# Kernel tuning notes

Hardware: AMD Instinct MI355X
Metric: run time of the kernel (lower is better)

## Reference

```python
import jax, jax.numpy as jnp
import numpy as np

SCALES = (128.0, 256.0, 512.0)
ASPECT = (0.5, 1.0, 2.0)
K = 9
NMS_THR = 0.7
PRE_NMS_TOPK = 10000
POST_NMS_TOPK = 2000
MIN_SIZE = 16.0

def conv2d(x, w, b, pad):
    out = jax.lax.conv_general_dilated(x, w, (1, 1), [(pad, pad), (pad, pad)], dimension_numbers=('NCHW', 'OIHW', 'NCHW'))
    return out + b[None, :, None, None]

def generate_anchors(grid_h, grid_w, dtype):
    # Faithful to source: shifts are grid indices, NOT multiplied by stride (source bug kept).
    scales = jnp.asarray(SCALES, dtype)
    ar = jnp.asarray(ASPECT, dtype)
    h_ratio = jnp.sqrt(ar)
    w_ratio = 1.0 / h_ratio
    ws = (w_ratio[:, None] * scales[None, :]).reshape(-1)
    hs = (h_ratio[:, None] * scales[None, :]).reshape(-1)
    base = jnp.round(jnp.stack([-ws, -hs, ws, hs], axis=1) / 2.0)  # (9,4)
    sy, sx = jnp.meshgrid(jnp.arange(grid_h), jnp.arange(grid_w), indexing='ij')
    sx = sx.reshape(-1).astype(dtype)
    sy = sy.reshape(-1).astype(dtype)
    shifts = jnp.stack([sx, sy, sx, sy], axis=1)  # (H*W,4)
    return (shifts[:, None, :] + base[None, :, :]).reshape(-1, 4)  # (H*W*9,4)

def decode(box_pred, anchors):
    w = anchors[:, 2] - anchors[:, 0]
    h = anchors[:, 3] - anchors[:, 1]
    cx = anchors[:, 0] + 0.5 * w
    cy = anchors[:, 1] + 0.5 * h
    dx, dy, dw, dh = box_pred[:, 0], box_pred[:, 1], box_pred[:, 2], box_pred[:, 3]
    pcx = dx * w + cx
    pcy = dy * h + cy
    pw = jnp.exp(dw) * w
    ph = jnp.exp(dh) * h
    return jnp.stack([pcx - 0.5 * pw, pcy - 0.5 * ph, pcx + 0.5 * pw, pcy + 0.5 * ph], axis=1)

def nms_keep(boxes, valid, thr):
    # Greedy NMS on score-descending boxes; invalid (small) boxes never kept nor suppress others.
    n = boxes.shape[0]
    x1, y1, x2, y2 = boxes[:, 0], boxes[:, 1], boxes[:, 2], boxes[:, 3]
    areas = (x2 - x1) * (y2 - y1)
    idx = jnp.arange(n)
    def body(i, keep):
        xx1 = jnp.maximum(x1, x1[i]); yy1 = jnp.maximum(y1, y1[i])
        xx2 = jnp.minimum(x2, x2[i]); yy2 = jnp.minimum(y2, y2[i])
        inter = jnp.maximum(xx2 - xx1, 0.0) * jnp.maximum(yy2 - yy1, 0.0)
        iou = inter / (areas + areas[i] - inter)
        suppress = (iou > thr) & (idx > i) & keep[i]
        return keep & (~suppress)
    return jax.lax.fori_loop(0, n, body, valid)

def filter_proposals(proposals, cls_scores, img_h, img_w):
    scores = jax.nn.sigmoid(cls_scores.reshape(-1))
    top_scores, top_idx = jax.lax.top_k(scores, PRE_NMS_TOPK)  # sorted descending
    props = proposals[top_idx]
    x1 = jnp.clip(props[:, 0], 0.0, img_w); y1 = jnp.clip(props[:, 1], 0.0, img_h)
    x2 = jnp.clip(props[:, 2], 0.0, img_w); y2 = jnp.clip(props[:, 3], 0.0, img_h)
    props = jnp.stack([x1, y1, x2, y2], axis=1)
    valid = ((x2 - x1) >= MIN_SIZE) & ((y2 - y1) >= MIN_SIZE)
    keep = jax.lax.stop_gradient(nms_keep(jax.lax.stop_gradient(props), valid, NMS_THR))
    masked = jnp.where(keep, top_scores, -1.0)
    final_scores, final_idx = jax.lax.top_k(masked, POST_NMS_TOPK)  # order = score-descending (matches post-NMS sort)
    final_props = props[final_idx]
    valid_out = final_scores > 0.0  # sigmoid scores > 0, padding = -1
    return jnp.where(valid_out[:, None], final_props, 0.0), jnp.where(valid_out, final_scores, 0.0)

def setup_inputs():
    key = jax.random.key(0)
    ks = jax.random.split(key, 8)
    C = 512; GH = GW = 50
    feat = jax.random.normal(ks[0], (1, C, GH, GW), jnp.float32)
    image = jnp.zeros((1, 3, 800, 800), jnp.float32)
    gt_boxes = jax.random.uniform(ks[1], (8, 4), jnp.float32) * 800.0
    w_rpn = jax.random.normal(ks[2], (C, C, 3, 3), jnp.float32) * 0.01
    b_rpn = jnp.zeros((C,), jnp.float32)
    w_cls = jax.random.normal(ks[3], (K, C, 1, 1), jnp.float32) * 0.01
    b_cls = jnp.zeros((K,), jnp.float32)
    w_reg = jax.random.normal(ks[4], (4 * K, C, 1, 1), jnp.float32) * 0.01
    b_reg = jnp.zeros((4 * K,), jnp.float32)
    return {"image": image, "feat": feat, "gt_boxes": gt_boxes, "w_rpn": w_rpn, "b_rpn": b_rpn, "w_cls": w_cls, "b_cls": b_cls, "w_reg": w_reg, "b_reg": b_reg}

def reference(image, feat, gt_boxes, w_rpn, b_rpn, w_cls, b_cls, w_reg, b_reg):
    rpn_feat = jax.nn.relu(conv2d(feat, w_rpn, b_rpn, 1))
    cls = conv2d(rpn_feat, w_cls, b_cls, 0)      # (B,9,H,W)
    reg = conv2d(rpn_feat, w_reg, b_reg, 0)      # (B,36,H,W)
    B, _, gh, gw = feat.shape
    anchors = generate_anchors(gh, gw, feat.dtype)
    # flatten to anchor ordering (h, w, k) matching generate_anchors
    cls_flat = jnp.transpose(cls, (0, 2, 3, 1)).reshape(-1)
    reg_flat = jnp.transpose(reg.reshape(B, K, 4, gh, gw), (0, 3, 4, 1, 2)).reshape(-1, 4)
    proposals = decode(reg_flat, anchors)
    img_h, img_w = float(image.shape[-2]), float(image.shape[-1])
    return filter_proposals(proposals, cls_flat, img_h, img_w)
```

## Files before the change

### kernel.cpp

```cpp
#include <hip/hip_runtime.h>
#include <cmath>
#include <cstdint>
#include <cstddef>

typedef unsigned long long u64;
typedef unsigned int u32;

#define NPX   2500
#define NANCH 22500
#define PRE_TOPK 10000
#define NWORDS 160

struct AnchorBase { float b[36]; };

typedef __attribute__((ext_vector_type(8))) short bf16x8;
typedef __attribute__((ext_vector_type(4))) float f32x4;

__device__ inline unsigned short f2bf(float f) {
    u32 u = __float_as_uint(f);
    u32 r = u + 0x7fffu + ((u >> 16) & 1u);
    return (unsigned short)(r >> 16);
}
__device__ inline float bf2f(unsigned short h) {
    return __uint_as_float(((u32)h) << 16);
}

__global__ __launch_bounds__(256) void kprep(const float* __restrict__ feat,
                                             const float* __restrict__ wr,
                                             unsigned short* __restrict__ xthi,
                                             unsigned short* __restrict__ xtlo,
                                             unsigned short* __restrict__ whi,
                                             unsigned short* __restrict__ wlo)
{
    __shared__ float sh[4608];
    int bid = blockIdx.x;
    int t = threadIdx.x;
    if (bid < 416) {
        float (*tile)[65] = (float(*)[65])sh;
        int gr = bid >> 3;
        int cc = bid & 7;
        int tx = t & 63, ty = t >> 6;
        int y = gr - 1;
        bool rowok = (gr >= 1) && (gr <= 50);
#pragma unroll
        for (int i = 0; i < 16; ++i) {
            int c = i * 4 + ty;
            tile[c][tx] = (rowok && tx < 50)
                        ? feat[(size_t)(cc * 64 + c) * NPX + y * 50 + tx] : 0.f;
        }
        __syncthreads();
#pragma unroll
        for (int i = 0; i < 16; ++i) {
            int xp = i * 4 + ty;
            int cell = gr * 64 + xp;
            bool ok = rowok && xp >= 1 && xp <= 50;
            float v = ok ? tile[tx][xp - 1] : 0.f;
            unsigned short hi = f2bf(v);
            xthi[(size_t)cell * 512 + cc * 64 + tx] = hi;
            xtlo[(size_t)cell * 512 + cc * 64 + tx] = f2bf(v - bf2f(hi));
        }
    } else {
        int oc = bid - 416;
        for (int j = t; j < 4608; j += 256) sh[j] = wr[(size_t)oc * 4608 + j];
        __syncthreads();
        for (int k = t; k < 4608; k += 256) {
            int c = k & 511, tap = k >> 9;
            float v = sh[c * 9 + tap];
            unsigned short hi = f2bf(v);
            whi[(size_t)oc * 4608 + k] = hi;
            wlo[(size_t)oc * 4608 + k] = f2bf(v - bf2f(hi));
        }
    }
}

__global__ __launch_bounds__(256) void k1m(const unsigned short* __restrict__ xthi,
                                           const unsigned short* __restrict__ xtlo,
                                           const unsigned short* __restrict__ whi,
                                           const unsigned short* __restrict__ wlo,
                                           float* __restrict__ pk,
                                           int cptLog, int cptm1, int cptMul, int niter)
{
    __shared__ __align__(16) unsigned short Ah[8192];
    __shared__ __align__(16) unsigned short Al[8192];
    __shared__ __align__(16) unsigned short Bh[4096];
    __shared__ __align__(16) unsigned short Bl[4096];

    int t = threadIdx.x;
    int lane = t & 63, wave = t >> 6;
    int wo = wave & 1, wp = wave >> 1;
    int ocb = blockIdx.x, pxb = blockIdx.y, bs = blockIdx.z;
    int q = lane >> 4, m = lane & 15;
    int c0base = bs * cptMul;

    int g  = t & 7;
    int r0 = t >> 3;
    int ocA[4];
    int cellB[2];
#pragma unroll
    for (int i = 0; i < 4; ++i) ocA[i] = ocb * 128 + r0 + 32 * i;
#pragma unroll
    for (int i = 0; i < 2; ++i) {
        int opx = pxb * 64 + r0 + 32 * i;
        cellB[i] = (opx < NPX) ? ((opx / 50) + 1) * 64 + (opx % 50) + 1 : 190;
    }

    f32x4 acc[8];
    f32x4 zf = {0.f, 0.f, 0.f, 0.f};
#pragma unroll
    for (int i = 0; i < 8; ++i) acc[i] = zf;

    for (int it = 0; it < niter; ++it) {
        int tap = it >> cptLog;
        int cw  = it & cptm1;
        int c0  = c0base + cw * 64;
        int t3  = (tap * 43) >> 7;
        int tapoff = (t3 - 1) * 64 + (tap - t3 * 3) - 1;
#pragma unroll
        for (int i = 0; i < 4; ++i) {
            int rl = r0 + 32 * i;
            int la = rl * 64 + g * 8;
            size_t ga = (size_t)ocA[i] * 4608 + tap * 512 + c0 + g * 8;
            *(bf16x8*)(Ah + la) = *(const bf16x8*)(whi + ga);
            *(bf16x8*)(Al + la) = *(const bf16x8*)(wlo + ga);
        }
#pragma unroll
        for (int i = 0; i < 2; ++i) {
            int rl = r0 + 32 * i;
            int la = rl * 64 + g * 8;
            size_t gb = (size_t)(cellB[i] + tapoff) * 512 + c0 + g * 8;
            *(bf16x8*)(Bh + la) = *(const bf16x8*)(xthi + gb);
            *(bf16x8*)(Bl + la) = *(const bf16x8*)(xtlo + gb);
        }
        __syncthreads();
#pragma unroll
        for (int ks = 0; ks < 2; ++ks) {
            bf16x8 fah[4], fal[4], fbh[2], fbl[2];
#pragma unroll
            for (int mt = 0; mt < 4; ++mt) {
                int off = (wo * 64 + mt * 16 + m) * 64 + ks * 32 + q * 8;
                fah[mt] = *(const bf16x8*)(Ah + off);
                fal[mt] = *(const bf16x8*)(Al + off);
            }
#pragma unroll
            for (int nt = 0; nt < 2; ++nt) {
                int off = (wp * 32 + nt * 16 + m) * 64 + ks * 32 + q * 8;
                fbh[nt] = *(const bf16x8*)(Bh + off);
                fbl[nt] = *(const bf16x8*)(Bl + off);
            }
#pragma unroll
            for (int mt = 0; mt < 4; ++mt)
#pragma unroll
                for (int nt = 0; nt < 2; ++nt) {
                    f32x4 a = acc[mt * 2 + nt];
                    a = __builtin_amdgcn_mfma_f32_16x16x32_bf16(fal[mt], fbh[nt], a, 0, 0, 0);
                    a = __builtin_amdgcn_mfma_f32_16x16x32_bf16(fah[mt], fbl[nt], a, 0, 0, 0);
                    a = __builtin_amdgcn_mfma_f32_16x16x32_bf16(fah[mt], fbh[nt], a, 0, 0, 0);
                    acc[mt * 2 + nt] = a;
                }
        }
        __syncthreads();
    }
#pragma unroll
    for (int mt = 0; mt < 4; ++mt)
#pragma unroll
        for (int nt = 0; nt < 2; ++nt)
#pragma unroll
            for (int r = 0; r < 4; ++r) {
                int oc = ocb * 128 + wo * 64 + mt * 16 + q * 4 + r;
                int px = pxb * 64 + wp * 32 + nt * 16 + m;
                pk[((size_t)bs * 512 + oc) * 2560 + px] = acc[mt * 2 + nt][r];
            }
}

__global__ __launch_bounds__(256) void k2a_heads(const float* __restrict__ pk, int ns,
                                                 const float* __restrict__ br,
                                                 const float* __restrict__ wcls,
                                                 const float* __restrict__ wreg,
                                                 float* __restrict__ part)
{
    __shared__ float vt[64 * 64];
    __shared__ float Wl[45 * 64];
    int t  = threadIdx.x;
    int pb = blockIdx.x;
    int s  = blockIdx.y;
    int cb = s * 64;
    for (int e = t; e < 45 * 64; e += 256) {
        int u = e >> 6, c = e & 63;
        Wl[e] = (u < 9) ? wcls[u * 512 + cb + c] : wreg[(u - 9) * 512 + cb + c];
    }
    int pxl = t & 63, ug = t >> 6;
    int px = pb * 64 + pxl;
    bool ok = px < NPX;
#pragma unroll
    for (int i = 0; i < 16; ++i) {
        int c = ug * 16 + i;
        float v = 0.f;
        if (ok) {
            size_t bidx = (size_t)(cb + c) * 2560 + px;
            v = br[cb + c];
            for (int ks = 0; ks < ns; ++ks) v += pk[(size_t)ks * 512 * 2560 + bidx];
            v = v > 0.f ? v : 0.f;
        }
        vt[c * 64 + pxl] = v;
    }
    __syncthreads();
    int ubase = ug * 12;
    int ulim  = (45 - ubase < 12) ? (45 - ubase) : 12;
    float acc[12];
#pragma unroll
    for (int j = 0; j < 12; ++j) acc[j] = 0.f;
    for (int c = 0; c < 64; ++c) {
        float v = vt[c * 64 + pxl];
#pragma unroll
        for (int j = 0; j < 12; ++j)
            acc[j] = fmaf(v, Wl[(ubase + j) * 64 + c], acc[j]);
    }
    if (ok) {
        for (int j = 0; j < ulim; ++j)
            part[((size_t)s * 45 + ubase + j) * NPX + px] = acc[j];
    }
}

__global__ __launch_bounds__(256) void k2b_decode(const float* __restrict__ part,
                                                  const float* __restrict__ bcls,
                                                  const float* __restrict__ breg,
                                                  AnchorBase ab,
                                                  float* __restrict__ score,
                                                  float* __restrict__ bx1, float* __restrict__ by1,
                                                  float* __restrict__ bx2, float* __restrict__ by2,
                                                  u32* __restrict__ valid,
                                                  u64* __restrict__ key)
{
    int id = blockIdx.x * 256 + threadIdx.x;
    if (id >= NANCH) return;
    int k  = id / NPX;
    int px = id - k * NPX;

    float z  = bcls[k];
    float d0 = breg[k * 4 + 0], d1 = breg[k * 4 + 1];
    float d2 = breg[k * 4 + 2], d3 = breg[k * 4 + 3];
#pragma unroll
    for (int s = 0; s < 8; ++s) {
        const float* p = part + (size_t)s * 45 * NPX;
        z  += p[(size_t)k * NPX + px];
        d0 += p[(size_t)(9 + k * 4 + 0) * NPX + px];
        d1 += p[(size_t)(9 + k * 4 + 1) * NPX + px];
        d2 += p[(size_t)(9 + k * 4 + 2) * NPX + px];
        d3 += p[(size_t)(9 + k * 4 + 3) * NPX + px];
    }
    float sc = 1.f / (1.f + expf(-z));

    int yy = px / 50, xx = px - (px / 50) * 50;
    float fx = (float)xx, fy = (float)yy;
    float ax1 = fx + ab.b[k * 4 + 0], ay1 = fy + ab.b[k * 4 + 1];
    float ax2 = fx + ab.b[k * 4 + 2], ay2 = fy + ab.b[k * 4 + 3];
    float aw = ax2 - ax1, ah = ay2 - ay1;
    float cx = ax1 + 0.5f * aw, cy = ay1 + 0.5f * ah;
    float pcx = d0 * aw + cx, pcy = d1 * ah + cy;
    float pw = expf(d2) * aw, ph = expf(d3) * ah;
    float x1 = pcx - 0.5f * pw, y1 = pcy - 0.5f * ph;
    float x2 = pcx + 0.5f * pw, y2 = pcy + 0.5f * ph;
    x1 = fminf(fmaxf(x1, 0.f), 800.f);
    y1 = fminf(fmaxf(y1, 0.f), 800.f);
    x2 = fminf(fmaxf(x2, 0.f), 800.f);
    y2 = fminf(fmaxf(y2, 0.f), 800.f);
    u32 v = ((x2 - x1) >= 16.f) && ((y2 - y1) >= 16.f);

    int f = px * 9 + k;
    score[f] = sc;
    bx1[f] = x1; by1[f] = y1; bx2[f] = x2; by2[f] = y2;
    valid[f] = v;
    u32 sb = __float_as_uint(sc);
    key[f] = ((u64)(~sb) << 32) | (u32)f;
}

__global__ __launch_bounds__(256) void k3a_rank(const u64* __restrict__ key,
                                                u32* __restrict__ rankp)
{
    __shared__ __align__(16) u64 sk[2250];
    int t  = threadIdx.x;
    int jb = blockIdx.y;
    for (int e = t; e < 2250; e += 256) sk[e] = key[jb * 2250 + e];
    __syncthreads();
    int i0 = blockIdx.x * 1024 + t;
    int i1 = i0 + 256, i2 = i0 + 512, i3 = i0 + 768;
    u64 k0 = (i0 < NANCH) ? key[i0] : 0ull;
    u64 k1 = (i1 < NANCH) ? key[i1] : 0ull;
    u64 k2 = (i2 < NANCH) ? key[i2] : 0ull;
    u64 k3 = (i3 < NANCH) ? key[i3] : 0ull;
    u32 c0 = 0, c1 = 0, c2 = 0, c3 = 0;
    const ulonglong2* sk2 = (const ulonglong2*)sk;
#pragma unroll 5
    for (int j = 0; j < 1125; ++j) {
        ulonglong2 v = sk2[j];
        c0 += (v.x < k0) ? 1u : 0u;  c0 += (v.y < k0) ? 1u : 0u;
        c1 += (v.x < k1) ? 1u : 0u;  c1 += (v.y < k1) ? 1u : 0u;
        c2 += (v.x < k2) ? 1u : 0u;  c2 += (v.y < k2) ? 1u : 0u;
        c3 += (v.x < k3) ? 1u : 0u;  c3 += (v.y < k3) ? 1u : 0u;
    }
    size_t base = (size_t)jb * NANCH;
    if (i0 < NANCH) rankp[base + i0] = c0;
    if (i1 < NANCH) rankp[base + i1] = c1;
    if (i2 < NANCH) rankp[base + i2] = c2;
    if (i3 < NANCH) rankp[base + i3] = c3;
}

__global__ __launch_bounds__(256) void k3b_gather(const u32* __restrict__ rankp,
                                                  const float* __restrict__ score,
                                                  const float* __restrict__ bx1, const float* __restrict__ by1,
                                                  const float* __restrict__ bx2, const float* __restrict__ by2,
                                                  const u32* __restrict__ valid,
                                                  float* __restrict__ sS,
                                                  float* __restrict__ sx1, float* __restrict__ sy1,
                                                  float* __restrict__ sx2, float* __restrict__ sy2,
                                                  float4* __restrict__ sbox4,
                                                  u32* __restrict__ sInv)
{
    int i = blockIdx.x * 256 + threadIdx.x;
    if (i >= NANCH) return;
    u32 r = 0;
#pragma unroll
    for (int c = 0; c < 10; ++c) r += rankp[(size_t)c * NANCH + i];
    if (r >= PRE_TOPK) return;
    float x1 = bx1[i], y1 = by1[i], x2 = bx2[i], y2 = by2[i];
    sS[r] = score[i];
    sx1[r] = x1; sy1[r] = y1; sx2[r] = x2; sy2[r] = y2;
    float4 b4; b4.x = x1; b4.y = y1; b4.z = x2; b4.w = y2;
    sbox4[r] = b4;
    sInv[r] = valid[i] ? 0u : 1u;
}

__global__ __launch_bounds__(256) void k4_mat(const float4* __restrict__ sbox4,
                                              u64* __restrict__ rows,
                                              u64* __restrict__ selfw)
{
    int t = threadIdx.x, lane = t & 63, wave = t >> 6;
    int i = blockIdx.x * 4 + wave;
    if (i >= PRE_TOPK) return;
    float4 bi = sbox4[i];
    float ai = (bi.z - bi.x) * (bi.w - bi.y);
    int wd  = i >> 6;
    int ish = i & 63;
    u64 diagmask = ~((2ull << ish) - 1ull);
    u64* rowp = rows + (size_t)i * NWORDS;
    for (int w = wd; w < 157; ++w) {
        float4 bj = sbox4[(w << 6) + lane];
        float xx1 = fmaxf(bi.x, bj.x);
        float yy1 = fmaxf(bi.y, bj.y);
        float xx2 = fminf(bi.z, bj.z);
        float yy2 = fminf(bi.w, bj.w);
        float iw = fmaxf(xx2 - xx1, 0.f);
        float ih = fmaxf(yy2 - yy1, 0.f);
        float inter = iw * ih;
        float aj = (bj.z - bj.x) * (bj.w - bj.y);
        float uni = ai + aj - inter;
        u64 b = __ballot(inter > 0.7f * uni);
        if (w == wd)  b &= diagmask;
        if (w == 156) b &= 0xFFFFull;
        if (lane == 0) {
            rowp[w] = b;
            if (w == wd) selfw[i] = b;
        }
    }
}

__global__ __launch_bounds__(64) void k5_scan(const u64* __restrict__ rows,
                                              const u64* __restrict__ selfw,
                                              const u32* __restrict__ sInv,
                                              const float* __restrict__ sS,
                                              const float* __restrict__ sx1, const float* __restrict__ sy1,
                                              const float* __restrict__ sx2, const float* __restrict__ sy2,
                                              float* __restrict__ out)
{
    __shared__ int keptList[2000];
    __shared__ int kcnt;
    int l = threadIdx.x;
    auto bw = [&](int w) -> u64 {
        const uint4* p = (const uint4*)(sInv + (size_t)w * 64);
        u64 v = 0;
#pragma unroll
        for (int j = 0; j < 16; ++j) {
            uint4 q = p[j];
            v |= ((u64)(q.x != 0) << (j * 4))     | ((u64)(q.y != 0) << (j * 4 + 1))
               | ((u64)(q.z != 0) << (j * 4 + 2)) | ((u64)(q.w != 0) << (j * 4 + 3));
        }
        return v;
    };
    u64 r0 = bw(l);
    u64 r1 = bw(64 + l);
    u64 r2 = (l < 32) ? bw(128 + l) : ~0ull;

    u64 cur[8], nxt[8];
#pragma unroll
    for (int k = 0; k < 8; ++k) cur[k] = selfw[(size_t)k * 64 + l];
#pragma unroll
    for (int k = 0; k < 8; ++k) {
        int ww = 8 + k;
        nxt[k] = (ww < 157) ? selfw[(size_t)ww * 64 + l] : 0ull;
    }

    int cnt = 0;
    bool done = false;
    for (int wg = 0; wg < 20; ++wg) {
#pragma unroll
        for (int ph = 0; ph < 8; ++ph) {
            int w = wg * 8 + ph;
            if (done || w > 156) continue;
            u64 swreg = cur[ph];
            int slot = w >> 6, owner = w & 63;
            u64 val = (slot == 0) ? r0 : (slot == 1) ? r1 : r2;
            u64 rw = __shfl(val, owner, 64);
            u64 wmask = (w == 156) ? 0xFFFFull : ~0ull;
            u64 av = (~rw) & wmask;
            u64 km = 0;
            while (av) {
                int b = __ffsll((unsigned long long)av) - 1;
                u64 sw = __shfl(swreg, b, 64);
                km |= 1ull << b;
                av &= ~(1ull << b);
                av &= ~sw;
            }
            u64 kk = km;
            while (kk) {
                int bsx[16];
                int nb = 0;
                while (kk && nb < 16) {
                    int b = __ffsll((unsigned long long)kk) - 1;
                    kk &= kk - 1;
                    bsx[nb++] = b;
                }
                u64 a0 = 0, a1 = 0, a2 = 0;
#pragma unroll
                for (int u = 0; u < 16; ++u) {
                    if (u < nb) {
                        int i = (w << 6) + bsx[u];
                        if (l == 0 && cnt + u < 2000) keptList[cnt + u] = i;
                        const u64* rp = rows + (size_t)i * NWORDS;
                        a0 |= rp[l];
                        a1 |= rp[64 + l];
                        if (l < 32) a2 |= rp[128 + l];
                    }
                }
                r0 |= a0; r1 |= a1; r2 |= a2;
                cnt += nb;
                if (cnt >= 2000) { done = true; break; }
            }
        }
        if (!done) {
            int base = (wg + 2) * 8;
#pragma unroll
            for (int k = 0; k < 8; ++k) cur[k] = nxt[k];
#pragma unroll
            for (int k = 0; k < 8; ++k) {
                int ww = base + k;
                nxt[k] = (ww < 157) ? selfw[(size_t)ww * 64 + l] : 0ull;
            }
        }
    }
    if (l == 0) kcnt = (cnt < 2000) ? cnt : 2000;
    __syncthreads();
    int K = kcnt;
    for (int r = l; r < 2000; r += 64) {
        if (r < K) {
            int j = keptList[r];
            out[r * 4 + 0] = sx1[j];
            out[r * 4 + 1] = sy1[j];
            out[r * 4 + 2] = sx2[j];
            out[r * 4 + 3] = sy2[j];
            out[8000 + r]  = sS[j];
        } else {
            out[r * 4 + 0] = 0.f; out[r * 4 + 1] = 0.f;
            out[r * 4 + 2] = 0.f; out[r * 4 + 3] = 0.f;
            out[8000 + r]  = 0.f;
        }
    }
}

extern "C" void kernel_launch(void* const* d_in, const int* in_sizes, int n_in,
                              void* d_out, int out_size, void* d_ws, size_t ws_size,
                              hipStream_t stream)
{
    (void)in_sizes; (void)n_in; (void)out_size;
    const float* feat = (const float*)d_in[1];
    const float* wrpn = (const float*)d_in[3];
    const float* brpn = (const float*)d_in[4];
    const float* wcls = (const float*)d_in[5];
    const float* bcls = (const float*)d_in[6];
    const float* wreg = (const float*)d_in[7];
    const float* breg = (const float*)d_in[8];
    float* out = (float*)d_out;

    int ns = (ws_size >= 58195968) ? 8 : (ws_size >= 37224448) ? 4 : 2;
    int cpt     = 8 / ns;
    int cptLog  = (ns == 2) ? 2 : (ns == 4) ? 1 : 0;
    int cptm1   = cpt - 1;
    int cptMul  = cpt * 64;
    int niter   = 9 * cpt;
    size_t pkB = (size_t)ns * 512 * 2560 * 4;

    char* ws = (char*)d_ws;
    float* pk = (float*)ws;
    unsigned short* Xthi = (unsigned short*)(ws + pkB);
    unsigned short* Xtlo = Xthi + (size_t)52 * 64 * 512;
    unsigned short* Whi  = (unsigned short*)(ws + pkB + 6815744);
    unsigned short* Wlo  = Whi + (size_t)512 * 4608;

    char* sm = ws + pkB;
    float* score = (float*)(sm + 0);
    float* bx1   = (float*)(sm + 90000);
    float* by1   = (float*)(sm + 180000);
    float* bx2   = (float*)(sm + 270000);
    float* by2   = (float*)(sm + 360000);
    u32*   valid = (u32*)  (sm + 450000);
    u64*   key   = (u64*)  (sm + 540000);
    u32*   rankp = (u32*)  (sm + 720000);
    float* sS    = (float*)(sm + 1620000);
    float* sx1   = (float*)(sm + 1660000);
    float* sy1   = (float*)(sm + 1700000);
    float* sx2   = (float*)(sm + 1740000);
    float* sy2   = (float*)(sm + 1780000);
    u32*   sInv  = (u32*)  (sm + 1820000);
    u64*   selfw = (u64*)  (sm + 1860960);
    float4* sbox4= (float4*)(sm + 1942880);
    float* part  = (float*)(sm + 2106720);
    u64*   rows  = (u64*)  (sm + 2106720);

    AnchorBase ab;
    {
        const float scales[3] = {128.f, 256.f, 512.f};
        const float aspect[3] = {0.5f, 1.f, 2.f};
        for (int ai = 0; ai < 3; ++ai) {
            float hr = sqrtf(aspect[ai]);
            float wratio = 1.0f / hr;
            for (int si = 0; si < 3; ++si) {
                float wsz = wratio * scales[si];
                float hsz = hr * scales[si];
                int a = ai * 3 + si;
                ab.b[a * 4 + 0] = rintf(-wsz / 2.0f);
                ab.b[a * 4 + 1] = rintf(-hsz / 2.0f);
                ab.b[a * 4 + 2] = rintf( wsz / 2.0f);
                ab.b[a * 4 + 3] = rintf( hsz / 2.0f);
            }
        }
    }

    kprep    <<<928, 256, 0, stream>>>(feat, wrpn, Xthi, Xtlo, Whi, Wlo);
    k1m      <<<dim3(4, 40, ns), 256, 0, stream>>>(Xthi, Xtlo, Whi, Wlo, pk,
                                                   cptLog, cptm1, cptMul, niter);
    k2a_heads<<<dim3(40, 8), 256, 0, stream>>>(pk, ns, brpn, wcls, wreg, part);
    k2b_decode<<<88, 256, 0, stream>>>(part, bcls, breg, ab, score, bx1, by1, bx2, by2, valid, key);
    k3a_rank <<<dim3(22, 10), 256, 0, stream>>>(key, rankp);
    k3b_gather<<<88, 256, 0, stream>>>(rankp, score, bx1, by1, bx2, by2, valid,
                                       sS, sx1, sy1, sx2, sy2, sbox4, sInv);
    hipMemsetAsync(rows, 0, (size_t)PRE_TOPK * NWORDS * 8, stream);
    k4_mat   <<<2500, 256, 0, stream>>>(sbox4, rows, selfw);
    k5_scan  <<<1, 64, 0, stream>>>(rows, selfw, sInv, sS, sx1, sy1, sx2, sy2, out);
}
```

Measured before the change: 374.5 us.

## Speculatively load suppression rows for candidate batches in greedy NMS scan

The single-wave greedy NMS loop no longer resolves the kept set within each 64-box word first and only then loads the kept boxes' suppression rows. It now gathers up to 32 candidate bits at once, issues their row loads and self-word shuffles together, resolves which candidates survive, and ORs in only the kept rows. The 8-deep group-wise self-word prefetch is replaced by a rolling 8-register window. This is meant to hide global load latency on the serial critical path, at the cost of extra loads for candidates that end up suppressed and higher register pressure from the 32-entry arrays.

```diff
diff --git a/kernel.cpp b/kernel.cpp
--- a/kernel.cpp
+++ b/kernel.cpp
@@ -390,72 +390,74 @@
     u64 r1 = bw(64 + l);
     u64 r2 = (l < 32) ? bw(128 + l) : ~0ull;
 
-    u64 cur[8], nxt[8];
-#pragma unroll
-    for (int k = 0; k < 8; ++k) cur[k] = selfw[(size_t)k * 64 + l];
-#pragma unroll
-    for (int k = 0; k < 8; ++k) {
-        int ww = 8 + k;
-        nxt[k] = (ww < 157) ? selfw[(size_t)ww * 64 + l] : 0ull;
-    }
+    u64 s0 = selfw[(size_t)0 * 64 + l];
+    u64 s1 = selfw[(size_t)1 * 64 + l];
+    u64 s2 = selfw[(size_t)2 * 64 + l];
+    u64 s3 = selfw[(size_t)3 * 64 + l];
+    u64 s4 = selfw[(size_t)4 * 64 + l];
+    u64 s5 = selfw[(size_t)5 * 64 + l];
+    u64 s6 = selfw[(size_t)6 * 64 + l];
+    u64 s7 = selfw[(size_t)7 * 64 + l];
 
     int cnt = 0;
     bool done = false;
-    for (int wg = 0; wg < 20; ++wg) {
-#pragma unroll
-        for (int ph = 0; ph < 8; ++ph) {
-            int w = wg * 8 + ph;
-            if (done || w > 156) continue;
-            u64 swreg = cur[ph];
-            int slot = w >> 6, owner = w & 63;
-            u64 val = (slot == 0) ? r0 : (slot == 1) ? r1 : r2;
-            u64 rw = __shfl(val, owner, 64);
-            u64 wmask = (w == 156) ? 0xFFFFull : ~0ull;
-            u64 av = (~rw) & wmask;
-            u64 km = 0;
-            while (av) {
-                int b = __ffsll((unsigned long long)av) - 1;
-                u64 sw = __shfl(swreg, b, 64);
-                km |= 1ull << b;
-                av &= ~(1ull << b);
-                av &= ~sw;
-            }
-            u64 kk = km;
-            while (kk) {
-                int bsx[16];
-                int nb = 0;
-                while (kk && nb < 16) {
-                    int b = __ffsll((unsigned long long)kk) - 1;
-                    kk &= kk - 1;
-                    bsx[nb++] = b;
+    for (int w = 0; w < 157; ++w) {
+        u64 swreg = s0;
+        s0 = s1; s1 = s2; s2 = s3; s3 = s4; s4 = s5; s5 = s6; s6 = s7;
+        s7 = (w + 8 < 157) ? selfw[(size_t)(w + 8) * 64 + l] : 0ull;
+
+        int slot = w >> 6, owner = w & 63;
+        u64 val = (slot == 0) ? r0 : (slot == 1) ? r1 : r2;
+        u64 rw = __shfl(val, owner, 64);
+        u64 wmask = (w == 156) ? 0xFFFFull : ~0ull;
+        u64 av = (~rw) & wmask;
+
+        while (av) {
+            int bs[32]; int nb = 0;
+            u64 tmp = av;
+#pragma unroll
+            for (int u = 0; u < 32; ++u) {
+                bs[u] = 0;
+                if (tmp) {
+                    bs[u] = __ffsll((unsigned long long)tmp) - 1;
+                    tmp &= tmp - 1;
+                    nb = u + 1;
                 }
-                u64 a0 = 0, a1 = 0, a2 = 0;
-#pragma unroll
-                for (int u = 0; u < 16; ++u) {
-                    if (u < nb) {
-                        int i = (w << 6) + bsx[u];
-                        if (l == 0 && cnt + u < 2000) keptList[cnt + u] = i;
-                        const u64* rp = rows + (size_t)i * NWORDS;
-                        a0 |= rp[l];
-                        a1 |= rp[64 + l];
-                        if (l < 32) a2 |= rp[128 + l];
-                    }
+            }
+            u64 A0[32], A1[32], A2[32], swv[32];
+#pragma unroll
+            for (int u = 0; u < 32; ++u) {
+                A0[u] = 0; A1[u] = 0; A2[u] = 0; swv[u] = 0;
+                if (u < nb) {
+                    const u64* rp = rows + (size_t)((w << 6) + bs[u]) * NWORDS;
+                    A0[u] = rp[l];
+                    A1[u] = rp[64 + l];
+                    if (l < 32) A2[u] = rp[128 + l];
+                    swv[u] = __shfl(swreg, bs[u], 64);
                 }
-                r0 |= a0; r1 |= a1; r2 |= a2;
-                cnt += nb;
-                if (cnt >= 2000) { done = true; break; }
-            }
-        }
-        if (!done) {
-            int base = (wg + 2) * 8;
-#pragma unroll
-            for (int k = 0; k < 8; ++k) cur[k] = nxt[k];
-#pragma unroll
-            for (int k = 0; k < 8; ++k) {
-                int ww = base + k;
-                nxt[k] = (ww < 157) ? selfw[(size_t)ww * 64 + l] : 0ull;
-            }
-        }
+            }
+            u64 kill = 0, km = 0;
+#pragma unroll
+            for (int u = 0; u < 32; ++u) {
+                if (u < nb) {
+                    u64 bit = 1ull << bs[u];
+                    if (!(kill & bit)) { km |= bit; kill |= swv[u]; }
+                }
+            }
+            av = tmp & ~kill;
+#pragma unroll
+            for (int u = 0; u < 32; ++u) {
+                if (u < nb && ((km >> bs[u]) & 1)) {
+                    if (l == 0 && cnt < 2000) keptList[cnt] = (w << 6) + bs[u];
+                    r0 |= A0[u];
+                    r1 |= A1[u];
+                    if (l < 32) r2 |= A2[u];
+                    ++cnt;
+                }
+            }
+            if (cnt >= 2000) { done = true; break; }
+        }
+        if (done) break;
     }
     if (l == 0) kcnt = (cnt < 2000) ? cnt : 2000;
     __syncthreads();
```

Result: slower. 453.1 us (+21.0%).
